# Kernel tuning notes

Hardware: AMD Instinct MI355X
Metric: run time of the kernel (lower is better)

## Reference

```python
import jax, jax.numpy as jnp
import numpy as np

VOCAB, EMB, SEQ, HID, TAGS, BATCH = 50000, 300, 256, 256, 50, 128


def _lstm_relu(x, Wx, Wh, b, reverse):
    """Keras LSTM with activation='relu', recurrent_activation='sigmoid'.
    x: [B,S,E] -> returns hidden states [B,S,H]. Gate order i,f,g,o (Keras)."""
    B = x.shape[0]
    H = Wh.shape[0]
    # Precompute input projections for all timesteps: [S,B,4H]
    xz = jnp.einsum('bse,eg->sbg', x, Wx) + b

    def step(carry, z_t):
        h, c = carry
        z = z_t + h @ Wh
        i, f, g, o = jnp.split(z, 4, axis=-1)
        c = jax.nn.sigmoid(f) * c + jax.nn.sigmoid(i) * jax.nn.relu(g)
        h = jax.nn.sigmoid(o) * jax.nn.relu(c)
        return (h, c), h

    h0 = jnp.zeros((B, H), x.dtype)
    _, hs = jax.lax.scan(step, (h0, h0), xz, reverse=reverse)  # hs: [S,B,H] in time order
    return jnp.swapaxes(hs, 0, 1)  # [B,S,H]


def setup_inputs() -> dict:
    key = jax.random.key(0)
    ks = jax.random.split(key, 10)
    s = 0.05  # small init keeps relu-LSTM states numerically tame
    return {
        'tokens': jax.random.randint(ks[0], (BATCH, SEQ), 0, VOCAB, dtype=jnp.int32),
        'emb':    jax.random.normal(ks[1], (VOCAB, EMB), jnp.float32) * s,
        'Wx_f':   jax.random.normal(ks[2], (EMB, 4 * HID), jnp.float32) * s,
        'Wh_f':   jax.random.normal(ks[3], (HID, 4 * HID), jnp.float32) * s,
        'b_f':    jnp.zeros((4 * HID,), jnp.float32),
        'Wx_b':   jax.random.normal(ks[4], (EMB, 4 * HID), jnp.float32) * s,
        'Wh_b':   jax.random.normal(ks[5], (HID, 4 * HID), jnp.float32) * s,
        'b_b':    jnp.zeros((4 * HID,), jnp.float32),
        'Wd':     jax.random.normal(ks[6], (2 * HID, TAGS), jnp.float32) * s,
        'bd':     jnp.zeros((TAGS,), jnp.float32),
    }


def reference(tokens, emb, Wx_f, Wh_f, b_f, Wx_b, Wh_b, b_b, Wd, bd):
    x = emb[tokens]                                  # [B,S,E] embedding lookup
    hf = _lstm_relu(x, Wx_f, Wh_f, b_f, reverse=False)
    hb = _lstm_relu(x, Wx_b, Wh_b, b_b, reverse=True)
    h = jnp.concatenate([hf, hb], axis=-1)           # [B,S,2H]
    # Dropout is identity at inference (Keras default training=False).
    return jax.nn.softmax(h @ Wd + bd, axis=-1)      # [B,S,TAGS]
```

## Files before the change

### kernel.cpp

```cpp
#include <hip/hip_runtime.h>
#include <stdint.h>

#define B_    128
#define S_    256
#define EMB_  300
#define HID_  256
#define TAGS_ 50
#define KP8   384
#define NROWS (B_ * S_)
#define GF    (4 * HID_)
#define NCOLS (2 * GF)

typedef __bf16 bf16x8 __attribute__((ext_vector_type(8)));
typedef float  f32x4  __attribute__((ext_vector_type(4)));
typedef unsigned int u32x4 __attribute__((ext_vector_type(4)));
typedef int    i32x8  __attribute__((ext_vector_type(8)));

__device__ __forceinline__ unsigned short f2bf(float f) {
    unsigned int u = __float_as_uint(f);
    unsigned int r = (u + 0x7fffu + ((u >> 16) & 1u)) >> 16;
    return (unsigned short)r;
}
__device__ __forceinline__ bf16x8 ldb8(const unsigned short* p) {
    u32x4 v = *reinterpret_cast<const u32x4*>(p);
    return __builtin_bit_cast(bf16x8, v);
}
__device__ __forceinline__ unsigned char f2fp8(float v) {
    int p = __builtin_amdgcn_cvt_pk_fp8_f32(v, 0.0f, 0, false);
    return (unsigned char)(p & 0xff);
}
__device__ __forceinline__ float sigf(float x) {
    return __builtin_amdgcn_rcpf(1.0f + __builtin_amdgcn_exp2f(x * -1.44269504f));
}
__device__ __forceinline__ float sel2(f32x4 v, int p) {
    return p ? v[1] : v[0];
}
__device__ __forceinline__ void gload_lds16(const void* g, void* l) {
    __builtin_amdgcn_global_load_lds(
        (const __attribute__((address_space(1))) void*)g,
        (__attribute__((address_space(3))) void*)l, 16, 0, 0);
}
__device__ __forceinline__ i32x8 mk8(u32x4 lo, u32x4 hi) {
    i32x8 r;
    r[0] = (int)lo[0]; r[1] = (int)lo[1]; r[2] = (int)lo[2]; r[3] = (int)lo[3];
    r[4] = (int)hi[0]; r[5] = (int)hi[1]; r[6] = (int)hi[2]; r[7] = (int)hi[3];
    return r;
}

__global__ void k_prep_all(const int* __restrict__ tokens, const float* __restrict__ emb,
                           const float* __restrict__ Wx_f, const float* __restrict__ Wx_b,
                           const float* __restrict__ Wd,
                           unsigned char* __restrict__ X8,
                           unsigned char* __restrict__ W8T,
                           unsigned short* __restrict__ WdT16) {
    int blk = blockIdx.x, k = threadIdx.x;
    if (blk < NROWS) {
        int b = blk & 127, s = blk >> 7;
        int tok = tokens[b * S_ + s];
        float v = (k < EMB_) ? emb[(long)tok * EMB_ + k] : 0.0f;
        X8[(long)blk * KP8 + k] = f2fp8(v);
    } else if (blk < NROWS + NCOLS) {
        int c = blk - NROWS;
        float v = 0.0f;
        if (k < EMB_) v = (c < GF) ? Wx_f[k * GF + c] : Wx_b[k * GF + (c - GF)];
        W8T[(long)c * KP8 + k] = f2fp8(v);
    } else {
        int e = (blk - NROWS - NCOLS) * 384 + k;
        if (e < 64 * 512) {
            int c = e >> 9, kk = e & 511;
            float v = (c < TAGS_) ? Wd[kk * TAGS_ + c] : 0.0f;
            WdT16[c * 512 + kk] = f2bf(v);
        }
    }
}

__global__ void k_prep_wh8(const float* __restrict__ Wh_f, const float* __restrict__ Wh_b,
                           unsigned char* __restrict__ WhP8) {
    int row = blockIdx.x;
    int k = threadIdx.x;
    int d = row >> 10, rr = row & 1023, gi = rr >> 8, j = rr & 255;
    const float* Wh = d ? Wh_b : Wh_f;
    WhP8[(long)row * 256 + k] = f2fp8(Wh[k * GF + gi * HID_ + j]);
}

__global__ __launch_bounds__(256) void k_gemm_xz(
    const unsigned char* __restrict__ X8, const unsigned char* __restrict__ W8T,
    const float* __restrict__ b_f, const float* __restrict__ b_b,
    unsigned long long* __restrict__ xzP) {
    __shared__ __align__(16) unsigned char A8s[2][128 * 128];
    __shared__ __align__(16) unsigned char B8s[2][128 * 128];
    int w = threadIdx.x >> 6, lane = threadIdx.x & 63;
    int quad = lane >> 4, l16 = lane & 15;
    int m0 = blockIdx.x * 128;
    int n0 = blockIdx.y * 128;

    int rlane = lane >> 3;
    int jpos  = lane & 7;
    int jsrc  = jpos ^ (rlane & 7);

    f32x4 acc[2][8];
#pragma unroll
    for (int mt = 0; mt < 2; ++mt)
#pragma unroll
        for (int nt = 0; nt < 8; ++nt) acc[mt][nt] = (f32x4){0.f, 0.f, 0.f, 0.f};

#define STAGE(ST, BUFI) do {                                                    \
    int k0_ = (ST) * 128;                                                       \
    _Pragma("unroll")                                                           \
    for (int i_ = 0; i_ < 4; ++i_) {                                            \
        int rb_ = (w * 4 + i_) * 8;                                             \
        int r_  = rb_ + rlane;                                                  \
        gload_lds16(X8 + (long)(m0 + r_) * KP8 + k0_ + jsrc * 16,               \
                    &A8s[BUFI][rb_ * 128]);                                     \
    }                                                                           \
    _Pragma("unroll")                                                           \
    for (int i_ = 0; i_ < 4; ++i_) {                                            \
        int rb_ = (w * 4 + i_) * 8;                                             \
        int r_  = rb_ + rlane;                                                  \
        gload_lds16(W8T + (long)(n0 + r_) * KP8 + k0_ + jsrc * 16,              \
                    &B8s[BUFI][rb_ * 128]);                                     \
    }                                                                           \
} while (0)

    STAGE(0, 0);
    __syncthreads();
#pragma unroll
    for (int st = 0; st < 3; ++st) {
        if (st < 2) STAGE(st + 1, (st + 1) & 1);
        int bufi = st & 1;
        i32x8 a[2], bb[8];
#pragma unroll
        for (int mt = 0; mt < 2; ++mt) {
            int mrow = w * 32 + mt * 16 + l16;
            int x_ = mrow & 7;
            u32x4 lo = *reinterpret_cast<const u32x4*>(
                &A8s[bufi][mrow * 128 + ((2 * quad) ^ x_) * 16]);
            u32x4 hi = *reinterpret_cast<const u32x4*>(
                &A8s[bufi][mrow * 128 + ((2 * quad + 1) ^ x_) * 16]);
            a[mt] = mk8(lo, hi);
        }
#pragma unroll
        for (int nt = 0; nt < 8; ++nt) {
            int nrow = nt * 16 + l16;
            int x_ = nrow & 7;
            u32x4 lo = *reinterpret_cast<const u32x4*>(
                &B8s[bufi][nrow * 128 + ((2 * quad) ^ x_) * 16]);
            u32x4 hi = *reinterpret_cast<const u32x4*>(
                &B8s[bufi][nrow * 128 + ((2 * quad + 1) ^ x_) * 16]);
            bb[nt] = mk8(lo, hi);
        }
#pragma unroll
        for (int mt = 0; mt < 2; ++mt)
#pragma unroll
            for (int nt = 0; nt < 8; ++nt)
#if __has_builtin(__builtin_amdgcn_mfma_scale_f32_16x16x128_f8f6f4)
                acc[mt][nt] = __builtin_amdgcn_mfma_scale_f32_16x16x128_f8f6f4(
                    a[mt], bb[nt], acc[mt][nt], 0, 0, 0, 0x7F, 0, 0x7F);
#else
                acc[mt][nt] = acc[mt][nt];
#endif
        __syncthreads();
    }
#undef STAGE

    int s = blockIdx.x;
#pragma unroll
    for (int mt = 0; mt < 2; ++mt) {
        int grp = w * 2 + mt;
#pragma unroll
        for (int nt = 0; nt < 8; ++nt) {
            int col = n0 + nt * 16 + l16;
            int dir = col >> 10, cc = col & 1023;
            int gate = cc >> 8, u16 = (cc & 255) >> 4;
            float bias = dir ? b_b[cc] : b_f[cc];
            unsigned long long pk = 0;
#pragma unroll
            for (int r = 0; r < 4; ++r)
                pk |= (unsigned long long)f2bf(acc[mt][nt][r] + bias) << (16 * r);
            long idx8 = ((long)(s * 16 + dir * 8 + grp)) * 4096 +
                        (gate * 16 + u16) * 64 + quad * 16 + l16;
            xzP[idx8] = pk;
        }
    }
}

__global__ __launch_bounds__(512, 2) void k_recurrence(
    const unsigned char* __restrict__ WhP8,
    const unsigned long long* __restrict__ xzP, unsigned short* __restrict__ hcat16) {
    __shared__ __align__(16) unsigned char lds[1152];
    int tid = threadIdx.x;
    int w = tid >> 6, lane = tid & 63, quad = lane >> 4, l16 = lane & 15;
    int blk = blockIdx.x;
    int d = blk >> 6, bg2 = blk & 63;
    int p = quad & 1;
    int cg = quad >> 1;
    int col = 16 * (2 * w + cg) + l16;
    int rp = l16 & 1;

    i32x8 wh8s[4][2][2];
#pragma unroll
    for (int gi = 0; gi < 4; ++gi)
#pragma unroll
        for (int cgi = 0; cgi < 2; ++cgi)
#pragma unroll
            for (int kt2 = 0; kt2 < 2; ++kt2) {
                const unsigned char* wp8 = WhP8 +
                    ((long)((d * 4 + gi) * 256 + 16 * (2 * w + cgi) + l16)) * 256 +
                    kt2 * 128 + quad * 32;
                i32x8 v = *reinterpret_cast<const i32x8*>(wp8);
                asm volatile("" : "+v"(v));
                wh8s[gi][cgi][kt2] = v;
            }

    float c2 = 0.f;

    const unsigned short* xzU = (const unsigned short*)xzP;
    int rowc = d * 8 + (bg2 >> 3);
    unsigned int laneoff = (unsigned)((2 * w + cg) * 256 +
                                      (((bg2 >> 1) & 3) * 16 + l16) * 4 +
                                      2 * (bg2 & 1) + p);

    unsigned short xzu[4];
    {
        int s0 = d ? 255 : 0;
        const unsigned short* ps = xzU + (unsigned long)(s0 * 16 + rowc) * 16384;
#pragma unroll
        for (int ga = 0; ga < 4; ++ga) xzu[ga] = ps[laneoff + ga * 4096];
    }

    for (int t = 0; t < 256; ++t) {
        int s = d ? (255 - t) : t;
        int pb = t & 1, cb = pb ^ 1;
        f32x4 acc8[4][2];
#pragma unroll
        for (int gi = 0; gi < 4; ++gi)
#pragma unroll
            for (int cgi = 0; cgi < 2; ++cgi) acc8[gi][cgi] = (f32x4){0.f, 0.f, 0.f, 0.f};

        if (t > 0) {
#pragma unroll
            for (int kt2 = 0; kt2 < 2; ++kt2) {
                i32x8 A8 = *reinterpret_cast<const i32x8*>(
                    lds + cb * 576 + rp * 288 + kt2 * 128 + quad * 32);
#pragma unroll
                for (int cgi = 0; cgi < 2; ++cgi)
#pragma unroll
                    for (int gi = 0; gi < 4; ++gi)
#if __has_builtin(__builtin_amdgcn_mfma_scale_f32_16x16x128_f8f6f4)
                        acc8[gi][cgi] = __builtin_amdgcn_mfma_scale_f32_16x16x128_f8f6f4(
                            A8, wh8s[gi][cgi][kt2], acc8[gi][cgi], 0, 0, 0, 0x7F, 0, 0x7F);
#else
                        acc8[gi][cgi] = acc8[gi][cgi];
#endif
            }
        }
        float xa0 = __uint_as_float((unsigned int)xzu[0] << 16);
        float xa1 = __uint_as_float((unsigned int)xzu[1] << 16);
        float xa2 = __uint_as_float((unsigned int)xzu[2] << 16);
        float xa3 = __uint_as_float((unsigned int)xzu[3] << 16);
        {
            int sn = d ? (s ? s - 1 : 0) : (s < 255 ? s + 1 : 255);
            const unsigned short* ps = xzU + (unsigned long)(sn * 16 + rowc) * 16384;
#pragma unroll
            for (int ga = 0; ga < 4; ++ga) xzu[ga] = ps[laneoff + ga * 4096];
        }
        float zi = (cg ? sel2(acc8[0][1], p) : sel2(acc8[0][0], p)) + xa0;
        float zf = (cg ? sel2(acc8[1][1], p) : sel2(acc8[1][0], p)) + xa1;
        float zg = (cg ? sel2(acc8[2][1], p) : sel2(acc8[2][0], p)) + xa2;
        float zo = (cg ? sel2(acc8[3][1], p) : sel2(acc8[3][0], p)) + xa3;
        float c = sigf(zf) * c2 + sigf(zi) * fmaxf(zg, 0.0f);
        c2 = c;
        float h = sigf(zo) * fmaxf(c, 0.0f);

        int p8 = __builtin_amdgcn_cvt_pk_fp8_f32(h, h, 0, false);
        *(lds + pb * 576 + p * 288 + col) = (unsigned char)(p8 & 0xff);
        hcat16[((long)(bg2 * 2 + p) * S_ + s) * 512 + d * HID_ + col] = f2bf(h);
        asm volatile("s_waitcnt lgkmcnt(0)\n\ts_barrier" ::: "memory");
    }
}

__global__ __launch_bounds__(256) void k_gemm_logits(
    const unsigned short* __restrict__ hcat16, const unsigned short* __restrict__ WdT16,
    const float* __restrict__ bd, float* __restrict__ out) {
    __shared__ __align__(16) unsigned short Asw[2][128 * 64];
    __shared__ __align__(16) unsigned short Bsw[2][64 * 64];
    int w = threadIdx.x >> 6, lane = threadIdx.x & 63;
    int quad = lane >> 4, l16 = lane & 15;
    int m0 = blockIdx.x * 128;
    int rlane = lane >> 3, jpos = lane & 7;
    int jsrc = jpos ^ (rlane & 7);

    f32x4 acc[2][4];
#pragma unroll
    for (int mt = 0; mt < 2; ++mt)
#pragma unroll
        for (int nt = 0; nt < 4; ++nt) acc[mt][nt] = (f32x4){0.f, 0.f, 0.f, 0.f};

#define STAGE3(ST, BUFI) do {                                                   \
    int k0_ = (ST) * 64;                                                        \
    _Pragma("unroll")                                                           \
    for (int i_ = 0; i_ < 4; ++i_) {                                            \
        int rb_ = (w * 4 + i_) * 8;                                             \
        int r_  = rb_ + rlane;                                                  \
        gload_lds16(hcat16 + (long)(m0 + r_) * 512 + k0_ + jsrc * 8,            \
                    &Asw[BUFI][rb_ * 64]);                                      \
    }                                                                           \
    _Pragma("unroll")                                                           \
    for (int i_ = 0; i_ < 2; ++i_) {                                            \
        int rb_ = (w * 2 + i_) * 8;                                             \
        int r_  = rb_ + rlane;                                                  \
        gload_lds16(WdT16 + (long)r_ * 512 + k0_ + jsrc * 8,                    \
                    &Bsw[BUFI][rb_ * 64]);                                      \
    }                                                                           \
} while (0)

    STAGE3(0, 0);
    __syncthreads();
#pragma unroll
    for (int st = 0; st < 8; ++st) {
        if (st < 7) STAGE3(st + 1, (st + 1) & 1);
        int bufi = st & 1;
#pragma unroll
        for (int ks = 0; ks < 2; ++ks) {
            bf16x8 a[2], bb[4];
#pragma unroll
            for (int mt = 0; mt < 2; ++mt) {
                int mrow = w * 32 + mt * 16 + l16;
                int jp = (ks * 4 + quad) ^ (l16 & 7);
                a[mt] = ldb8(&Asw[bufi][mrow * 64 + jp * 8]);
            }
#pragma unroll
            for (int nt = 0; nt < 4; ++nt) {
                int nrow = nt * 16 + l16;
                int jp = (ks * 4 + quad) ^ (l16 & 7);
                bb[nt] = ldb8(&Bsw[bufi][nrow * 64 + jp * 8]);
            }
#pragma unroll
            for (int mt = 0; mt < 2; ++mt)
#pragma unroll
                for (int nt = 0; nt < 4; ++nt)
                    acc[mt][nt] = __builtin_amdgcn_mfma_f32_16x16x32_bf16(a[mt], bb[nt], acc[mt][nt], 0, 0, 0);
        }
        __syncthreads();
    }
#undef STAGE3

#pragma unroll
    for (int mt = 0; mt < 2; ++mt) {
#pragma unroll
        for (int r = 0; r < 4; ++r) {
            int row = m0 + w * 32 + mt * 16 + quad * 4 + r;
            float vv[4];
            float mx = -3.0e38f;
#pragma unroll
            for (int nt = 0; nt < 4; ++nt) {
                int cl = nt * 16 + l16;
                float tv = (cl < TAGS_) ? (acc[mt][nt][r] + bd[cl]) : -3.0e38f;
                vv[nt] = tv;
                mx = fmaxf(mx, tv);
            }
#pragma unroll
            for (int off = 8; off >= 1; off >>= 1) mx = fmaxf(mx, __shfl_xor(mx, off, 64));
            float sum = 0.f;
#pragma unroll
            for (int nt = 0; nt < 4; ++nt) {
                int cl = nt * 16 + l16;
                float e = (cl < TAGS_) ? __expf(vv[nt] - mx) : 0.0f;
                vv[nt] = e;
                sum += e;
            }
#pragma unroll
            for (int off = 8; off >= 1; off >>= 1) sum += __shfl_xor(sum, off, 64);
            float rs = __builtin_amdgcn_rcpf(sum);
#pragma unroll
            for (int nt = 0; nt < 4; ++nt) {
                int cl = nt * 16 + l16;
                if (cl < TAGS_) out[(long)row * TAGS_ + cl] = vv[nt] * rs;
            }
        }
    }
}

extern "C" void kernel_launch(void* const* d_in, const int* in_sizes, int n_in,
                              void* d_out, int out_size, void* d_ws, size_t ws_size,
                              hipStream_t stream) {
    (void)in_sizes; (void)n_in; (void)out_size; (void)ws_size;
    const int*   tokens = (const int*)  d_in[0];
    const float* emb    = (const float*)d_in[1];
    const float* Wx_f   = (const float*)d_in[2];
    const float* Wh_f   = (const float*)d_in[3];
    const float* b_f    = (const float*)d_in[4];
    const float* Wx_b   = (const float*)d_in[5];
    const float* Wh_b   = (const float*)d_in[6];
    const float* b_b    = (const float*)d_in[7];
    const float* Wd     = (const float*)d_in[8];
    const float* bd     = (const float*)d_in[9];
    float* out = (float*)d_out;

    uint8_t* w = (uint8_t*)d_ws;
    unsigned char*  X8     = (unsigned char*)(w);
    unsigned char*  W8T    = (unsigned char*)(w + 12582912);
    unsigned char*  WhP8   = (unsigned char*)(w);
    unsigned short* WdT16  = (unsigned short*)(w + 22282240);
    unsigned long long* xzP = (unsigned long long*)(w + 22347776);
    unsigned short* hcat16 = (unsigned short*)(w + 156565504);

    k_prep_all  <<<dim3(NROWS + NCOLS + 86), dim3(KP8), 0, stream>>>(
        tokens, emb, Wx_f, Wx_b, Wd, X8, W8T, WdT16);
    k_gemm_xz   <<<dim3(256, 16),   dim3(256),  0, stream>>>(X8, W8T, b_f, b_b, xzP);
    k_prep_wh8  <<<dim3(2048),      dim3(256),  0, stream>>>(Wh_f, Wh_b, WhP8);
    k_recurrence<<<dim3(128),       dim3(512),  0, stream>>>(WhP8, xzP, hcat16);
    k_gemm_logits<<<dim3(256),      dim3(256),  0, stream>>>(hcat16, WdT16, bd, out);
}
```

Baseline: 401.7 us.

## Store xz projections in fp8 and fold Wh prep into prep kernel

The input-projection GEMM now writes its biased outputs as packed fp8 instead of bf16. The recurrence loads single bytes and converts them to f32, halving xz memory traffic and footprint. The separate Wh fp8 prep kernel is merged into the combined prep kernel as extra blocks, removing one launch. WhP8 moves to its own workspace region. The trade is reduced precision on the gate pre-activations, which may affect accuracy.

After: 382.9 us. 1.05x faster.

```diff
diff --git a/kernel.cpp b/kernel.cpp
--- a/kernel.cpp
+++ b/kernel.cpp
@@ -29,6 +29,16 @@
     int p = __builtin_amdgcn_cvt_pk_fp8_f32(v, 0.0f, 0, false);
     return (unsigned char)(p & 0xff);
 }
+__device__ __forceinline__ float fp8_to_f32(unsigned int b) {
+#if __has_builtin(__builtin_amdgcn_cvt_f32_fp8)
+    return __builtin_amdgcn_cvt_f32_fp8((int)b, 0);
+#else
+    unsigned int s = (b >> 7) & 1u, e = (b >> 3) & 15u, m = b & 7u;
+    float mag = e ? __uint_as_float(((e + 120u) << 23) | (m << 20))
+                  : (float)m * 0.001953125f;
+    return s ? -mag : mag;
+#endif
+}
 __device__ __forceinline__ float sigf(float x) {
     return __builtin_amdgcn_rcpf(1.0f + __builtin_amdgcn_exp2f(x * -1.44269504f));
 }
@@ -50,9 +60,11 @@
 __global__ void k_prep_all(const int* __restrict__ tokens, const float* __restrict__ emb,
                            const float* __restrict__ Wx_f, const float* __restrict__ Wx_b,
                            const float* __restrict__ Wd,
+                           const float* __restrict__ Wh_f, const float* __restrict__ Wh_b,
                            unsigned char* __restrict__ X8,
                            unsigned char* __restrict__ W8T,
-                           unsigned short* __restrict__ WdT16) {
+                           unsigned short* __restrict__ WdT16,
+                           unsigned char* __restrict__ WhP8) {
     int blk = blockIdx.x, k = threadIdx.x;
     if (blk < NROWS) {
         int b = blk & 127, s = blk >> 7;
@@ -64,29 +76,25 @@
         float v = 0.0f;
         if (k < EMB_) v = (c < GF) ? Wx_f[k * GF + c] : Wx_b[k * GF + (c - GF)];
         W8T[(long)c * KP8 + k] = f2fp8(v);
-    } else {
+    } else if (blk < NROWS + NCOLS + 86) {
         int e = (blk - NROWS - NCOLS) * 384 + k;
         if (e < 64 * 512) {
             int c = e >> 9, kk = e & 511;
             float v = (c < TAGS_) ? Wd[kk * TAGS_ + c] : 0.0f;
             WdT16[c * 512 + kk] = f2bf(v);
         }
-    }
-}
-
-__global__ void k_prep_wh8(const float* __restrict__ Wh_f, const float* __restrict__ Wh_b,
-                           unsigned char* __restrict__ WhP8) {
-    int row = blockIdx.x;
-    int k = threadIdx.x;
-    int d = row >> 10, rr = row & 1023, gi = rr >> 8, j = rr & 255;
-    const float* Wh = d ? Wh_b : Wh_f;
-    WhP8[(long)row * 256 + k] = f2fp8(Wh[k * GF + gi * HID_ + j]);
+    } else if (k < 256) {
+        int row = blk - (NROWS + NCOLS + 86);
+        int d = row >> 10, rr = row & 1023, gi = rr >> 8, j = rr & 255;
+        const float* Wh = d ? Wh_b : Wh_f;
+        WhP8[(long)row * 256 + k] = f2fp8(Wh[k * GF + gi * HID_ + j]);
+    }
 }
 
 __global__ __launch_bounds__(256) void k_gemm_xz(
     const unsigned char* __restrict__ X8, const unsigned char* __restrict__ W8T,
     const float* __restrict__ b_f, const float* __restrict__ b_b,
-    unsigned long long* __restrict__ xzP) {
+    unsigned int* __restrict__ xz32) {
     __shared__ __align__(16) unsigned char A8s[2][128 * 128];
     __shared__ __align__(16) unsigned char B8s[2][128 * 128];
     int w = threadIdx.x >> 6, lane = threadIdx.x & 63;
@@ -173,20 +181,20 @@
             int dir = col >> 10, cc = col & 1023;
             int gate = cc >> 8, u16 = (cc & 255) >> 4;
             float bias = dir ? b_b[cc] : b_f[cc];
-            unsigned long long pk = 0;
-#pragma unroll
-            for (int r = 0; r < 4; ++r)
-                pk |= (unsigned long long)f2bf(acc[mt][nt][r] + bias) << (16 * r);
+            int t0 = __builtin_amdgcn_cvt_pk_fp8_f32(
+                acc[mt][nt][0] + bias, acc[mt][nt][1] + bias, 0, false);
+            int t1 = __builtin_amdgcn_cvt_pk_fp8_f32(
+                acc[mt][nt][2] + bias, acc[mt][nt][3] + bias, t0, true);
             long idx8 = ((long)(s * 16 + dir * 8 + grp)) * 4096 +
                         (gate * 16 + u16) * 64 + quad * 16 + l16;
-            xzP[idx8] = pk;
+            xz32[idx8] = (unsigned int)t1;
         }
     }
 }
 
 __global__ __launch_bounds__(512, 2) void k_recurrence(
     const unsigned char* __restrict__ WhP8,
-    const unsigned long long* __restrict__ xzP, unsigned short* __restrict__ hcat16) {
+    const unsigned char* __restrict__ xz8, unsigned short* __restrict__ hcat16) {
     __shared__ __align__(16) unsigned char lds[1152];
     int tid = threadIdx.x;
     int w = tid >> 6, lane = tid & 63, quad = lane >> 4, l16 = lane & 15;
@@ -214,18 +222,17 @@
 
     float c2 = 0.f;
 
-    const unsigned short* xzU = (const unsigned short*)xzP;
     int rowc = d * 8 + (bg2 >> 3);
     unsigned int laneoff = (unsigned)((2 * w + cg) * 256 +
                                       (((bg2 >> 1) & 3) * 16 + l16) * 4 +
                                       2 * (bg2 & 1) + p);
 
-    unsigned short xzu[4];
+    unsigned int xzu[4];
     {
         int s0 = d ? 255 : 0;
-        const unsigned short* ps = xzU + (unsigned long)(s0 * 16 + rowc) * 16384;
-#pragma unroll
-        for (int ga = 0; ga < 4; ++ga) xzu[ga] = ps[laneoff + ga * 4096];
+        const unsigned char* ps = xz8 + (unsigned long)(s0 * 16 + rowc) * 16384 + laneoff;
+#pragma unroll
+        for (int ga = 0; ga < 4; ++ga) xzu[ga] = ps[ga * 4096];
     }
 
     for (int t = 0; t < 256; ++t) {
@@ -254,15 +261,15 @@
 #endif
             }
         }
-        float xa0 = __uint_as_float((unsigned int)xzu[0] << 16);
-        float xa1 = __uint_as_float((unsigned int)xzu[1] << 16);
-        float xa2 = __uint_as_float((unsigned int)xzu[2] << 16);
-        float xa3 = __uint_as_float((unsigned int)xzu[3] << 16);
+        float xa0 = fp8_to_f32(xzu[0]);
+        float xa1 = fp8_to_f32(xzu[1]);
+        float xa2 = fp8_to_f32(xzu[2]);
+        float xa3 = fp8_to_f32(xzu[3]);
         {
             int sn = d ? (s ? s - 1 : 0) : (s < 255 ? s + 1 : 255);
-            const unsigned short* ps = xzU + (unsigned long)(sn * 16 + rowc) * 16384;
-#pragma unroll
-            for (int ga = 0; ga < 4; ++ga) xzu[ga] = ps[laneoff + ga * 4096];
+            const unsigned char* ps = xz8 + (unsigned long)(sn * 16 + rowc) * 16384 + laneoff;
+#pragma unroll
+            for (int ga = 0; ga < 4; ++ga) xzu[ga] = ps[ga * 4096];
         }
         float zi = (cg ? sel2(acc8[0][1], p) : sel2(acc8[0][0], p)) + xa0;
         float zf = (cg ? sel2(acc8[1][1], p) : sel2(acc8[1][0], p)) + xa1;
@@ -400,15 +407,15 @@
     uint8_t* w = (uint8_t*)d_ws;
     unsigned char*  X8     = (unsigned char*)(w);
     unsigned char*  W8T    = (unsigned char*)(w + 12582912);
-    unsigned char*  WhP8   = (unsigned char*)(w);
     unsigned short* WdT16  = (unsigned short*)(w + 22282240);
-    unsigned long long* xzP = (unsigned long long*)(w + 22347776);
+    unsigned char*  xz8    = (unsigned char*)(w + 22347776);
+    unsigned char*  WhP8   = (unsigned char*)(w + 89456640);
     unsigned short* hcat16 = (unsigned short*)(w + 156565504);
 
-    k_prep_all  <<<dim3(NROWS + NCOLS + 86), dim3(KP8), 0, stream>>>(
-        tokens, emb, Wx_f, Wx_b, Wd, X8, W8T, WdT16);
-    k_gemm_xz   <<<dim3(256, 16),   dim3(256),  0, stream>>>(X8, W8T, b_f, b_b, xzP);
-    k_prep_wh8  <<<dim3(2048),      dim3(256),  0, stream>>>(Wh_f, Wh_b, WhP8);
-    k_recurrence<<<dim3(128),       dim3(512),  0, stream>>>(WhP8, xzP, hcat16);
+    k_prep_all  <<<dim3(NROWS + NCOLS + 86 + 2048), dim3(KP8), 0, stream>>>(
+        tokens, emb, Wx_f, Wx_b, Wd, Wh_f, Wh_b, X8, W8T, WdT16, WhP8);
+    k_gemm_xz   <<<dim3(256, 16),   dim3(256),  0, stream>>>(
+        X8, W8T, b_f, b_b, (unsigned int*)xz8);
+    k_recurrence<<<dim3(128),       dim3(512),  0, stream>>>(WhP8, xz8, hcat16);
     k_gemm_logits<<<dim3(256),      dim3(256),  0, stream>>>(hcat16, WdT16, bd, out);
 }
```
